# Kernel tuning notes

Hardware: AMD Instinct MI355X
Metric: run time of the kernel (lower is better)

The kernel has to match this reference:

```python
import jax, jax.numpy as jnp
import numpy as np

E = 1024  # embedding_size
H = 16    # num_heads
D = E // H  # head_size = 64
SCALE = 1.0 / np.sqrt(np.float32(E))  # NOTE: original scales by sqrt(embedding_size), not head_size


def setup_inputs() -> dict:
    key = jax.random.key(0)
    ks = jax.random.split(key, 11)
    B, S = 2, 2048
    init = 1.0 / np.sqrt(np.float32(E))
    inp = {
        'q': jax.random.normal(ks[0], (B, S, E), dtype=jnp.float32),
        'k': jax.random.normal(ks[1], (B, S, E), dtype=jnp.float32),
        'v': jax.random.normal(ks[2], (B, S, E), dtype=jnp.float32),
        'wq': jax.random.normal(ks[3], (E, E), dtype=jnp.float32) * init,
        'bq': jax.random.normal(ks[4], (E,), dtype=jnp.float32) * init,
        'wk': jax.random.normal(ks[5], (E, E), dtype=jnp.float32) * init,
        'bk': jax.random.normal(ks[6], (E,), dtype=jnp.float32) * init,
        'wv': jax.random.normal(ks[7], (E, E), dtype=jnp.float32) * init,
        'bv': jax.random.normal(ks[8], (E,), dtype=jnp.float32) * init,
        'wo': jax.random.normal(ks[9], (E, E), dtype=jnp.float32) * init,
        'bo': jax.random.normal(ks[10], (E,), dtype=jnp.float32) * init,
    }
    return inp


def reference(q, k, v, wq, bq, wk, bk, wv, bv, wo, bo):
    S = q.shape[1]
    # Linear projections (torch Linear: x @ W.T + b)
    qp = (q @ wq.T + bq).reshape(-1, H, S, D)  # faithful raw view, not transpose
    kp = (k @ wk.T + bk).reshape(-1, H, S, D)
    vp = (v @ wv.T + bv).reshape(-1, H, S, D)
    # scores / sqrt(embedding_size) -- faithful to original (uses E, not D)
    scores = jnp.einsum('bhqd,bhkd->bhqk', qp, kp) * SCALE
    attn = jax.nn.softmax(scores, axis=-1)  # [B,H,S,S]
    out = jnp.einsum('bhqk,bhkd->bhqd', attn, vp)  # [B,H,S,D]
    out = out.reshape(-1, S, E)
    # dropout is eval-mode identity
    return out @ wo.T + bo
```

## Files before the change

kernel.cpp:

```cpp
#include <hip/hip_runtime.h>
#include <hip/hip_bf16.h>
#include <cstdint>


typedef __bf16 bf16_t;
typedef bf16_t bf16x8 __attribute__((ext_vector_type(8)));
typedef bf16_t bf16x4 __attribute__((ext_vector_type(4)));
typedef float  f32x4  __attribute__((ext_vector_type(4)));
typedef float  f32x16 __attribute__((ext_vector_type(16)));
typedef unsigned int u32;
typedef u32 u32x2 __attribute__((ext_vector_type(2)));

#define MFMA16(a, b, c) __builtin_amdgcn_mfma_f32_16x16x32_bf16((a), (b), (c), 0, 0, 0)
#define MFMA32(a, b, c) __builtin_amdgcn_mfma_f32_32x32x16_bf16((a), (b), (c), 0, 0, 0)

#define GLOAD_LDS16(gptr, lptr)                                                      \
  __builtin_amdgcn_global_load_lds(                                                  \
      (const __attribute__((address_space(1))) void*)(gptr),                         \
      (__attribute__((address_space(3))) void*)(lptr), 16, 0, 0)

namespace {
constexpr int kS = 2048, kE = 1024, kD = 64;
constexpr int kM = 4096;
constexpr float kQScale = 0.03125f;
constexpr float kL2E = 1.44269504088896f;
}

__device__ inline u32 pkbf(float a, float b) {
  u32 r;
  asm("v_cvt_pk_bf16_f32 %0, %1, %2" : "=v"(r) : "v"(a), "v"(b));
  return r;
}

__device__ inline bf16x8 make_pfrag(float v0, float v1, float v2, float v3,
                                    float v4, float v5, float v6, float v7) {
  u32 A0 = pkbf(v0, v1), A1 = pkbf(v2, v3);
  u32 B0 = pkbf(v4, v5), B1 = pkbf(v6, v7);
  u32x2 r0 = __builtin_amdgcn_permlane32_swap(A0, B0, false, false);
  u32x2 r1 = __builtin_amdgcn_permlane32_swap(A1, B1, false, false);
  union { u32 w[4]; bf16x8 v; } u;
  u.w[0] = r0[0]; u.w[1] = r1[0]; u.w[2] = r0[1]; u.w[3] = r1[1];
  return u.v;
}

__global__ void cvt_batch(const float* __restrict__ s0, const float* __restrict__ s1,
                          const float* __restrict__ s2, const float* __restrict__ s3,
                          bf16_t* __restrict__ d0, bf16_t* __restrict__ d1,
                          bf16_t* __restrict__ d2, bf16_t* __restrict__ d3, int n4) {
  const float* s; bf16_t* d;
  switch (blockIdx.y) {
    case 0:  s = s0; d = d0; break;
    case 1:  s = s1; d = d1; break;
    case 2:  s = s2; d = d2; break;
    default: s = s3; d = d3; break;
  }
  int stride = gridDim.x * blockDim.x;
  for (int i = blockIdx.x * blockDim.x + threadIdx.x; i < n4; i += stride) {
    float4 v = reinterpret_cast<const float4*>(s)[i];
    bf16x4 o;
    o[0] = (bf16_t)v.x; o[1] = (bf16_t)v.y; o[2] = (bf16_t)v.z; o[3] = (bf16_t)v.w;
    reinterpret_cast<bf16x4*>(d)[i] = o;
  }
}

__global__ __launch_bounds__(256, 2)
void gemm_qkv(const bf16_t* __restrict__ qb, const bf16_t* __restrict__ kb,
              const bf16_t* __restrict__ vb, const bf16_t* __restrict__ W,
              const float* __restrict__ bq, const float* __restrict__ bk,
              const float* __restrict__ bv,
              bf16_t* __restrict__ Qp, bf16_t* __restrict__ Kp, bf16_t* __restrict__ Vp) {
  constexpr int K = kE, BK = 64;
  __shared__ __align__(16) bf16_t As[128 * BK];
  __shared__ __align__(16) bf16_t Bs[128 * BK];
  const int tid = threadIdx.x, lane = tid & 63, wave = tid >> 6;
  const int fr = lane & 15, fg = lane >> 4;
  const int region = blockIdx.x >> 3;
  const int bm = blockIdx.y * 128, bn = blockIdx.x * 128;
  const int bnl = (blockIdx.x & 7) * 128;
  const bf16_t* A = region == 0 ? qb : region == 1 ? kb : vb;
  const float* bias = region == 0 ? bq : region == 1 ? bk : bv;
  bf16_t* Cp = region == 0 ? Qp : region == 1 ? Kp : Vp;
  const float scale = region == 0 ? kQScale : 1.0f;
  const int wr = (wave >> 1) * 64, wc = (wave & 1) * 64;
  f32x4 acc[4][4] = {};
  for (int k0 = 0; k0 < K; k0 += BK) {
#pragma unroll
    for (int c = 0; c < 4; ++c) {
      int lin = c * 256 + tid, row = lin >> 3, ch = lin & 7, sch = ch ^ (row & 7);
      GLOAD_LDS16(A + (size_t)(bm + row) * K + k0 + sch * 8, (char*)As + lin * 16);
    }
#pragma unroll
    for (int c = 0; c < 4; ++c) {
      int lin = c * 256 + tid, row = lin >> 3, ch = lin & 7, sch = ch ^ (row & 7);
      GLOAD_LDS16(W + (size_t)(bn + row) * K + k0 + sch * 8, (char*)Bs + lin * 16);
    }
    __syncthreads();
#pragma unroll
    for (int kk = 0; kk < 2; ++kk) {
      bf16x8 af[4], bfv[4];
#pragma unroll
      for (int i = 0; i < 4; ++i) {
        int row = wr + i * 16 + fr;
        int ch = (kk * 4 + fg) ^ (row & 7);
        af[i] = *reinterpret_cast<const bf16x8*>((const char*)As + row * 128 + ch * 16);
      }
#pragma unroll
      for (int j = 0; j < 4; ++j) {
        int row = wc + j * 16 + fr;
        int ch = (kk * 4 + fg) ^ (row & 7);
        bfv[j] = *reinterpret_cast<const bf16x8*>((const char*)Bs + row * 128 + ch * 16);
      }
#pragma unroll
      for (int i = 0; i < 4; ++i)
#pragma unroll
        for (int j = 0; j < 4; ++j)
          acc[i][j] = MFMA16(af[i], bfv[j], acc[i][j]);
    }
    __syncthreads();
  }
#pragma unroll
  for (int i = 0; i < 4; ++i)
#pragma unroll
    for (int j = 0; j < 4; ++j) {
      int coll = bnl + wc + j * 16 + fr;
      float bvv = bias[coll];
#pragma unroll
      for (int r = 0; r < 4; ++r) {
        int row = bm + wr + i * 16 + fg * 4 + r;
        Cp[(size_t)row * kE + coll] = (bf16_t)((acc[i][j][r] + bvv) * scale);
      }
    }
}

__global__ __launch_bounds__(256, 2)
void gemm_out(const bf16_t* __restrict__ A, const bf16_t* __restrict__ Bm,
              const float* __restrict__ bias, float* __restrict__ Cout) {
  constexpr int K = kE, BK = 64;
  __shared__ __align__(16) bf16_t As[128 * BK];
  __shared__ __align__(16) bf16_t Bs[64 * BK];
  const int tid = threadIdx.x, lane = tid & 63, wave = tid >> 6;
  const int fr = lane & 15, fg = lane >> 4;
  const int bm = blockIdx.y * 128, bn = blockIdx.x * 64;
  const int wr = wave * 32;
  f32x4 acc[2][4] = {};
  for (int k0 = 0; k0 < K; k0 += BK) {
#pragma unroll
    for (int c = 0; c < 4; ++c) {
      int lin = c * 256 + tid, row = lin >> 3, ch = lin & 7, sch = ch ^ (row & 7);
      GLOAD_LDS16(A + (size_t)(bm + row) * K + k0 + sch * 8, (char*)As + lin * 16);
    }
#pragma unroll
    for (int c = 0; c < 2; ++c) {
      int lin = c * 256 + tid, row = lin >> 3, ch = lin & 7, sch = ch ^ (row & 7);
      GLOAD_LDS16(Bm + (size_t)(bn + row) * K + k0 + sch * 8, (char*)Bs + lin * 16);
    }
    __syncthreads();
#pragma unroll
    for (int kk = 0; kk < 2; ++kk) {
      bf16x8 af[2], bfv[4];
#pragma unroll
      for (int i = 0; i < 2; ++i) {
        int row = wr + i * 16 + fr;
        int ch = (kk * 4 + fg) ^ (row & 7);
        af[i] = *reinterpret_cast<const bf16x8*>((const char*)As + row * 128 + ch * 16);
      }
#pragma unroll
      for (int j = 0; j < 4; ++j) {
        int row = bn - bn + j * 16 + fr;
        int ch = (kk * 4 + fg) ^ (row & 7);
        bfv[j] = *reinterpret_cast<const bf16x8*>((const char*)Bs + row * 128 + ch * 16);
      }
#pragma unroll
      for (int i = 0; i < 2; ++i)
#pragma unroll
        for (int j = 0; j < 4; ++j)
          acc[i][j] = MFMA16(af[i], bfv[j], acc[i][j]);
    }
    __syncthreads();
  }
#pragma unroll
  for (int i = 0; i < 2; ++i)
#pragma unroll
    for (int j = 0; j < 4; ++j) {
      int col = bn + j * 16 + fr;
      float bvv = bias[col];
#pragma unroll
      for (int r = 0; r < 4; ++r) {
        int row = bm + wr + i * 16 + fg * 4 + r;
        Cout[(size_t)row * kE + col] = acc[i][j][r] + bvv;
      }
    }
}

__global__ __launch_bounds__(256)
void vtranspose(const bf16_t* __restrict__ Vp, bf16_t* __restrict__ VpT) {
  __shared__ __align__(16) bf16_t T[256 * 64];
  const int tid = threadIdx.x;
  const size_t hb = (size_t)blockIdx.y * (kS * kD);
  const bf16_t* src = Vp + hb + (size_t)blockIdx.x * 256 * kD;
  bf16_t* dst = VpT + hb + blockIdx.x * 256;
#pragma unroll
  for (int c = 0; c < 8; ++c) {
    int lin = c * 256 + tid;
    int row = lin >> 3, ch = lin & 7;
    bf16x8 v = *reinterpret_cast<const bf16x8*>(src + row * kD + ch * 8);
    *reinterpret_cast<bf16x8*>((char*)T + row * 128 + ((ch ^ ((row >> 3) & 7)) * 16)) = v;
  }
  __syncthreads();
#pragma unroll
  for (int c = 0; c < 8; ++c) {
    int lin = c * 256 + tid;
    int d = lin >> 5, kc = lin & 31;
    bf16x8 o;
#pragma unroll
    for (int e = 0; e < 8; ++e) {
      int s = kc * 8 + e;
      o[e] = *reinterpret_cast<const bf16_t*>(
          (const char*)T + s * 128 + (((d >> 3) ^ ((s >> 3) & 7)) * 16) + (d & 7) * 2);
    }
    *reinterpret_cast<bf16x8*>(dst + (size_t)d * kS + kc * 8) = o;
  }
}

__global__ __launch_bounds__(256, 3)
void attn_fwd(const bf16_t* __restrict__ Qp, const bf16_t* __restrict__ Kp,
              const bf16_t* __restrict__ VpT, bf16_t* __restrict__ Op) {
  __shared__ __align__(16) char smem[32768];
  const int tid = threadIdx.x, lane = tid & 63, wave = tid >> 6;
  const int ql = lane & 31, hi = lane >> 5;
  const int newb = (blockIdx.x & 7) * 64 + (blockIdx.x >> 3);
  const int head = newb >> 4, qt = newb & 15;
  const size_t hbase = (size_t)head * (kS * kD);
  const int q0 = qt * 128 + wave * 32;

  bf16x8 qf[4];
#pragma unroll
  for (int ct = 0; ct < 4; ++ct)
    qf[ct] = *reinterpret_cast<const bf16x8*>(
        Qp + hbase + (size_t)(q0 + ql) * kD + ct * 16 + hi * 8);

  float m = -3.0e38f, Lp = 0.0f;
  f32x16 o0 = {}, o1 = {};

  {
    const bf16_t* Kt = Kp + hbase;
    const bf16_t* Vt = VpT + hbase;
#pragma unroll
    for (int c = 0; c < 2; ++c) {
      int lin = c * 256 + tid, row = lin >> 3, ch = lin & 7, sch = ch ^ (row & 7);
      GLOAD_LDS16(Kt + row * kD + sch * 8, smem + lin * 16);
      GLOAD_LDS16(Vt + (size_t)row * kS + sch * 8, smem + 8192 + lin * 16);
    }
  }

  for (int kt = 0; kt < kS / 64; ++kt) {
    __syncthreads();
    const int cb = (kt & 1) * 16384;
    if (kt + 1 < kS / 64) {
      const int nb = ((kt + 1) & 1) * 16384;
      const bf16_t* Kt = Kp + hbase + (size_t)(kt + 1) * 64 * kD;
      const bf16_t* Vt = VpT + hbase + (kt + 1) * 64;
#pragma unroll
      for (int c = 0; c < 2; ++c) {
        int lin = c * 256 + tid, row = lin >> 3, ch = lin & 7, sch = ch ^ (row & 7);
        GLOAD_LDS16(Kt + row * kD + sch * 8, smem + nb + lin * 16);
        GLOAD_LDS16(Vt + (size_t)row * kS + sch * 8, smem + nb + 8192 + lin * 16);
      }
    }

    f32x16 s0 = {}, s1 = {};
#pragma unroll
    for (int ct = 0; ct < 4; ++ct) {
      bf16x8 k0 = *reinterpret_cast<const bf16x8*>(
          smem + cb + ql * 128 + (((2 * ct + hi) ^ (ql & 7)) * 16));
      bf16x8 k1 = *reinterpret_cast<const bf16x8*>(
          smem + cb + (32 + ql) * 128 + (((2 * ct + hi) ^ (ql & 7)) * 16));
      s0 = MFMA32(k0, qf[ct], s0);
      s1 = MFMA32(k1, qf[ct], s1);
    }

    float t0 = -3.0e38f, t1 = -3.0e38f, t2 = -3.0e38f, t3 = -3.0e38f;
#pragma unroll
    for (int r = 0; r < 16; r += 4) {
      t0 = fmaxf(t0, fmaxf(s0[r], s0[r + 1])); t1 = fmaxf(t1, fmaxf(s0[r + 2], s0[r + 3]));
      t2 = fmaxf(t2, fmaxf(s1[r], s1[r + 1])); t3 = fmaxf(t3, fmaxf(s1[r + 2], s1[r + 3]));
    }
    float tm = fmaxf(fmaxf(t0, t1), fmaxf(t2, t3));
    tm = fmaxf(tm, __shfl_xor(tm, 32));
    if (!__all(tm <= m + 8.0f)) {
      float mn = fmaxf(m, tm);
      float rs = __builtin_amdgcn_exp2f((m - mn) * kL2E);
      m = mn; Lp *= rs;
#pragma unroll
      for (int r = 0; r < 16; ++r) { o0[r] *= rs; o1[r] *= rs; }
    }
    const float ml = m * kL2E;
    float a0 = 0.f, a1 = 0.f;
#pragma unroll
    for (int r = 0; r < 16; ++r) {
      s0[r] = __builtin_amdgcn_exp2f(__builtin_fmaf(s0[r], kL2E, -ml));
      s1[r] = __builtin_amdgcn_exp2f(__builtin_fmaf(s1[r], kL2E, -ml));
      a0 += s0[r]; a1 += s1[r];
    }
    Lp += a0 + a1;

    bf16x8 pf[4];
    pf[0] = make_pfrag(s0[0], s0[1], s0[2], s0[3], s0[4], s0[5], s0[6], s0[7]);
    pf[1] = make_pfrag(s0[8], s0[9], s0[10], s0[11], s0[12], s0[13], s0[14], s0[15]);
    pf[2] = make_pfrag(s1[0], s1[1], s1[2], s1[3], s1[4], s1[5], s1[6], s1[7]);
    pf[3] = make_pfrag(s1[8], s1[9], s1[10], s1[11], s1[12], s1[13], s1[14], s1[15]);

#pragma unroll
    for (int ks = 0; ks < 4; ++ks) {
      bf16x8 v0 = *reinterpret_cast<const bf16x8*>(
          smem + cb + 8192 + ql * 128 + (((2 * ks + hi) ^ (ql & 7)) * 16));
      bf16x8 v1 = *reinterpret_cast<const bf16x8*>(
          smem + cb + 8192 + (32 + ql) * 128 + (((2 * ks + hi) ^ (ql & 7)) * 16));
      o0 = MFMA32(v0, pf[ks], o0);
      o1 = MFMA32(v1, pf[ks], o1);
    }
  }

  float L = Lp + __shfl_xor(Lp, 32);
  float inv = 1.0f / L;
#pragma unroll
  for (int r = 0; r < 16; ++r) { o0[r] *= inv; o1[r] *= inv; }
  const int wb = wave * 4096;
#pragma unroll
  for (int c = 0; c < 4; ++c) {
    {
      u32 w0 = pkbf(o0[4 * c + 0], o0[4 * c + 1]);
      u32 w1 = pkbf(o0[4 * c + 2], o0[4 * c + 3]);
      int d0 = 8 * c + 4 * hi;
      int byte = (wb + ql * 128 + d0 * 2) ^ ((ql & 7) << 4);
      *reinterpret_cast<u32x2*>(smem + byte) = (u32x2){w0, w1};
    }
    {
      u32 w0 = pkbf(o1[4 * c + 0], o1[4 * c + 1]);
      u32 w1 = pkbf(o1[4 * c + 2], o1[4 * c + 3]);
      int d0 = 32 + 8 * c + 4 * hi;
      int byte = (wb + ql * 128 + d0 * 2) ^ ((ql & 7) << 4);
      *reinterpret_cast<u32x2*>(smem + byte) = (u32x2){w0, w1};
    }
  }
  asm volatile("s_waitcnt lgkmcnt(0)" ::: "memory");
  __builtin_amdgcn_sched_barrier(0);
#pragma unroll
  for (int it = 0; it < 4; ++it) {
    int lin = it * 64 + lane;
    int qr = lin >> 3, ch = lin & 7;
    int byte = wb + qr * 128 + ((ch * 16) ^ ((qr & 7) << 4));
    bf16x8 vrow = *reinterpret_cast<const bf16x8*>(smem + byte);
    *reinterpret_cast<bf16x8*>(Op + hbase + (size_t)(q0 + qr) * kD + ch * 8) = vrow;
  }
}

extern "C" void kernel_launch(void* const* d_in, const int* in_sizes, int n_in,
                              void* d_out, int out_size, void* d_ws, size_t ws_size,
                              hipStream_t stream) {
  (void)in_sizes; (void)n_in; (void)out_size; (void)ws_size;
  const float* q  = (const float*)d_in[0];
  const float* k  = (const float*)d_in[1];
  const float* v  = (const float*)d_in[2];
  const float* wq = (const float*)d_in[3];
  const float* bq = (const float*)d_in[4];
  const float* wk = (const float*)d_in[5];
  const float* bk = (const float*)d_in[6];
  const float* wv = (const float*)d_in[7];
  const float* bv = (const float*)d_in[8];
  const float* wo = (const float*)d_in[9];
  const float* bo = (const float*)d_in[10];
  float* out = (float*)d_out;

  char* ws = (char*)d_ws;
  const size_t MB = 1ull << 20;
  bf16_t* qb   = (bf16_t*)(ws +  0 * MB);
  bf16_t* kb   = (bf16_t*)(ws +  8 * MB);
  bf16_t* vb   = (bf16_t*)(ws + 16 * MB);
  bf16_t* wqkv = (bf16_t*)(ws + 24 * MB);
  bf16_t* wob  = (bf16_t*)(ws + 30 * MB);
  bf16_t* Qp   = (bf16_t*)(ws + 32 * MB);
  bf16_t* Kp   = (bf16_t*)(ws + 40 * MB);
  bf16_t* Vp   = (bf16_t*)(ws + 48 * MB);
  bf16_t* Opb  = (bf16_t*)(ws + 56 * MB);
  bf16_t* VpT  = (bf16_t*)(ws +  0 * MB);

  const int nQKV4 = (kM * kE) / 4;
  const int nW4 = (kE * kE) / 4;
  cvt_batch<<<dim3(512, 3), 256, 0, stream>>>(q, k, v, v, qb, kb, vb, vb, nQKV4);
  cvt_batch<<<dim3(128, 4), 256, 0, stream>>>(wq, wk, wv, wo, wqkv, wqkv + 1048576,
                                              wqkv + 2097152, wob, nW4);

  gemm_qkv<<<dim3(24, 32), 256, 0, stream>>>(qb, kb, vb, wqkv, bq, bk, bv, Qp, Kp, Vp);

  vtranspose<<<dim3(kS / 256, 32), 256, 0, stream>>>(Vp, VpT);

  attn_fwd<<<dim3(512), 256, 0, stream>>>(Qp, Kp, VpT, Opb);

  gemm_out<<<dim3(16, 32), 256, 0, stream>>>(Opb, wob, bo, out);
}
```

Measured before the change: 128.1 us.

## Software-pipeline attention so PV of previous tile overlaps QK of current

Restructures the attention main loop so the P·V MFMAs for tile kt-1 are issued alongside the Q·K MFMAs for tile kt, with P fragments ping-ponged between two register sets and K/V staged in separate double buffers. The goal is to hide softmax exp and permute latency behind matrix work, and s_setprio raises priority around the MFMA section. Blocks shrink to two waves (64 query rows) with twice as many blocks, and the cross-half shuffles become permlane32_swap. The trade-offs are more register pressure from the extra P fragments, a loose launch-bounds hint, and more K reloads across the larger block count.

```diff
diff --git a/kernel.cpp b/kernel.cpp
--- a/kernel.cpp
+++ b/kernel.cpp
@@ -41,6 +41,17 @@
   union { u32 w[4]; bf16x8 v; } u;
   u.w[0] = r0[0]; u.w[1] = r1[0]; u.w[2] = r0[1]; u.w[3] = r1[1];
   return u.v;
+}
+
+__device__ inline float xhalf_max(float x) {
+  u32 xu = __builtin_bit_cast(u32, x);
+  u32x2 r = __builtin_amdgcn_permlane32_swap(xu, xu, false, false);
+  return fmaxf(__builtin_bit_cast(float, r[0]), __builtin_bit_cast(float, r[1]));
+}
+__device__ inline float xhalf_sum(float x) {
+  u32 xu = __builtin_bit_cast(u32, x);
+  u32x2 r = __builtin_amdgcn_permlane32_swap(xu, xu, false, false);
+  return __builtin_bit_cast(float, r[0]) + __builtin_bit_cast(float, r[1]);
 }
 
 __global__ void cvt_batch(const float* __restrict__ s0, const float* __restrict__ s1,
@@ -166,7 +177,7 @@
       }
 #pragma unroll
       for (int j = 0; j < 4; ++j) {
-        int row = bn - bn + j * 16 + fr;
+        int row = j * 16 + fr;
         int ch = (kk * 4 + fg) ^ (row & 7);
         bfv[j] = *reinterpret_cast<const bf16x8*>((const char*)Bs + row * 128 + ch * 16);
       }
@@ -222,16 +233,94 @@
   }
 }
 
-__global__ __launch_bounds__(256, 3)
+#define ATTN_BODY(KT, PFW, PFR, DOPV, STAGEK)                                        \
+  {                                                                                  \
+    __syncthreads();                                                                 \
+    const int cb = ((KT) & 1) * 8192;                                                \
+    const int vbR = 16384 + ((((KT) + 1) & 1) * 8192);                               \
+    if (STAGEK) {                                                                    \
+      const bf16_t* Ktp = Kp + hbase + (size_t)((KT) + 1) * 64 * kD;                 \
+      const int nb = (((KT) + 1) & 1) * 8192;                                        \
+      _Pragma("unroll")                                                              \
+      for (int c = 0; c < 4; ++c) {                                                  \
+        int lin = c * 128 + tid, row = lin >> 3, ch = lin & 7, sch = ch ^ (row & 7); \
+        GLOAD_LDS16(Ktp + row * kD + sch * 8, smem + nb + lin * 16);                 \
+      }                                                                              \
+    }                                                                                \
+    {                                                                                \
+      const bf16_t* Vtp = VpT + hbase + (KT) * 64;                                   \
+      const int vbW = 16384 + (((KT) & 1) * 8192);                                   \
+      _Pragma("unroll")                                                              \
+      for (int c = 0; c < 4; ++c) {                                                  \
+        int lin = c * 128 + tid, row = lin >> 3, ch = lin & 7, sch = ch ^ (row & 7); \
+        GLOAD_LDS16(Vtp + (size_t)row * kS + sch * 8, smem + vbW + lin * 16);        \
+      }                                                                              \
+    }                                                                                \
+    f32x16 s0 = {}, s1 = {};                                                         \
+    __builtin_amdgcn_s_setprio(1);                                                   \
+    _Pragma("unroll")                                                                \
+    for (int ct = 0; ct < 4; ++ct) {                                                 \
+      bf16x8 k0 = *reinterpret_cast<const bf16x8*>(                                  \
+          smem + cb + ql * 128 + (((2 * ct + hi) ^ (ql & 7)) * 16));                 \
+      bf16x8 k1 = *reinterpret_cast<const bf16x8*>(                                  \
+          smem + cb + (32 + ql) * 128 + (((2 * ct + hi) ^ (ql & 7)) * 16));          \
+      s0 = MFMA32(k0, qf[ct], s0);                                                   \
+      s1 = MFMA32(k1, qf[ct], s1);                                                   \
+    }                                                                                \
+    if (DOPV) {                                                                      \
+      _Pragma("unroll")                                                              \
+      for (int ks = 0; ks < 4; ++ks) {                                               \
+        bf16x8 v0 = *reinterpret_cast<const bf16x8*>(                                \
+            smem + vbR + ql * 128 + (((2 * ks + hi) ^ (ql & 7)) * 16));              \
+        bf16x8 v1 = *reinterpret_cast<const bf16x8*>(                                \
+            smem + vbR + (32 + ql) * 128 + (((2 * ks + hi) ^ (ql & 7)) * 16));       \
+        o0 = MFMA32(v0, PFR[ks], o0);                                                \
+        o1 = MFMA32(v1, PFR[ks], o1);                                                \
+      }                                                                              \
+    }                                                                                \
+    __builtin_amdgcn_s_setprio(0);                                                   \
+    float t0 = -3.0e38f, t1 = -3.0e38f, t2 = -3.0e38f, t3 = -3.0e38f;                \
+    _Pragma("unroll")                                                                \
+    for (int r = 0; r < 16; r += 4) {                                                \
+      t0 = fmaxf(t0, fmaxf(s0[r], s0[r + 1]));                                       \
+      t1 = fmaxf(t1, fmaxf(s0[r + 2], s0[r + 3]));                                   \
+      t2 = fmaxf(t2, fmaxf(s1[r], s1[r + 1]));                                       \
+      t3 = fmaxf(t3, fmaxf(s1[r + 2], s1[r + 3]));                                   \
+    }                                                                                \
+    float tm = fmaxf(fmaxf(t0, t1), fmaxf(t2, t3));                                  \
+    tm = xhalf_max(tm);                                                              \
+    if (!__all(tm <= m + 8.0f)) {                                                    \
+      float mn = fmaxf(m, tm);                                                       \
+      float rs = __builtin_amdgcn_exp2f((m - mn) * kL2E);                            \
+      m = mn; Lp *= rs;                                                              \
+      _Pragma("unroll")                                                              \
+      for (int r = 0; r < 16; ++r) { o0[r] *= rs; o1[r] *= rs; }                     \
+    }                                                                                \
+    const float ml = m * kL2E;                                                       \
+    float a0 = 0.f, a1 = 0.f;                                                        \
+    _Pragma("unroll")                                                                \
+    for (int r = 0; r < 16; ++r) {                                                   \
+      s0[r] = __builtin_amdgcn_exp2f(__builtin_fmaf(s0[r], kL2E, -ml));              \
+      s1[r] = __builtin_amdgcn_exp2f(__builtin_fmaf(s1[r], kL2E, -ml));              \
+      a0 += s0[r]; a1 += s1[r];                                                      \
+    }                                                                                \
+    Lp += a0 + a1;                                                                   \
+    PFW[0] = make_pfrag(s0[0], s0[1], s0[2], s0[3], s0[4], s0[5], s0[6], s0[7]);     \
+    PFW[1] = make_pfrag(s0[8], s0[9], s0[10], s0[11], s0[12], s0[13], s0[14], s0[15]);\
+    PFW[2] = make_pfrag(s1[0], s1[1], s1[2], s1[3], s1[4], s1[5], s1[6], s1[7]);     \
+    PFW[3] = make_pfrag(s1[8], s1[9], s1[10], s1[11], s1[12], s1[13], s1[14], s1[15]);\
+  }
+
+__global__ __launch_bounds__(128, 2)
 void attn_fwd(const bf16_t* __restrict__ Qp, const bf16_t* __restrict__ Kp,
               const bf16_t* __restrict__ VpT, bf16_t* __restrict__ Op) {
   __shared__ __align__(16) char smem[32768];
   const int tid = threadIdx.x, lane = tid & 63, wave = tid >> 6;
   const int ql = lane & 31, hi = lane >> 5;
-  const int newb = (blockIdx.x & 7) * 64 + (blockIdx.x >> 3);
-  const int head = newb >> 4, qt = newb & 15;
+  const int newb = ((int)blockIdx.x & 7) * 128 + ((int)blockIdx.x >> 3);
+  const int head = newb >> 5, qt = newb & 31;
   const size_t hbase = (size_t)head * (kS * kD);
-  const int q0 = qt * 128 + wave * 32;
+  const int q0 = qt * 64 + wave * 32;
 
   bf16x8 qf[4];
 #pragma unroll
@@ -241,87 +330,38 @@
 
   float m = -3.0e38f, Lp = 0.0f;
   f32x16 o0 = {}, o1 = {};
+  bf16x8 pfA[4], pfB[4];
 
   {
-    const bf16_t* Kt = Kp + hbase;
-    const bf16_t* Vt = VpT + hbase;
-#pragma unroll
-    for (int c = 0; c < 2; ++c) {
-      int lin = c * 256 + tid, row = lin >> 3, ch = lin & 7, sch = ch ^ (row & 7);
-      GLOAD_LDS16(Kt + row * kD + sch * 8, smem + lin * 16);
-      GLOAD_LDS16(Vt + (size_t)row * kS + sch * 8, smem + 8192 + lin * 16);
-    }
-  }
-
-  for (int kt = 0; kt < kS / 64; ++kt) {
-    __syncthreads();
-    const int cb = (kt & 1) * 16384;
-    if (kt + 1 < kS / 64) {
-      const int nb = ((kt + 1) & 1) * 16384;
-      const bf16_t* Kt = Kp + hbase + (size_t)(kt + 1) * 64 * kD;
-      const bf16_t* Vt = VpT + hbase + (kt + 1) * 64;
-#pragma unroll
-      for (int c = 0; c < 2; ++c) {
-        int lin = c * 256 + tid, row = lin >> 3, ch = lin & 7, sch = ch ^ (row & 7);
-        GLOAD_LDS16(Kt + row * kD + sch * 8, smem + nb + lin * 16);
-        GLOAD_LDS16(Vt + (size_t)row * kS + sch * 8, smem + nb + 8192 + lin * 16);
-      }
-    }
-
-    f32x16 s0 = {}, s1 = {};
-#pragma unroll
-    for (int ct = 0; ct < 4; ++ct) {
-      bf16x8 k0 = *reinterpret_cast<const bf16x8*>(
-          smem + cb + ql * 128 + (((2 * ct + hi) ^ (ql & 7)) * 16));
-      bf16x8 k1 = *reinterpret_cast<const bf16x8*>(
-          smem + cb + (32 + ql) * 128 + (((2 * ct + hi) ^ (ql & 7)) * 16));
-      s0 = MFMA32(k0, qf[ct], s0);
-      s1 = MFMA32(k1, qf[ct], s1);
-    }
-
-    float t0 = -3.0e38f, t1 = -3.0e38f, t2 = -3.0e38f, t3 = -3.0e38f;
-#pragma unroll
-    for (int r = 0; r < 16; r += 4) {
-      t0 = fmaxf(t0, fmaxf(s0[r], s0[r + 1])); t1 = fmaxf(t1, fmaxf(s0[r + 2], s0[r + 3]));
-      t2 = fmaxf(t2, fmaxf(s1[r], s1[r + 1])); t3 = fmaxf(t3, fmaxf(s1[r + 2], s1[r + 3]));
-    }
-    float tm = fmaxf(fmaxf(t0, t1), fmaxf(t2, t3));
-    tm = fmaxf(tm, __shfl_xor(tm, 32));
-    if (!__all(tm <= m + 8.0f)) {
-      float mn = fmaxf(m, tm);
-      float rs = __builtin_amdgcn_exp2f((m - mn) * kL2E);
-      m = mn; Lp *= rs;
-#pragma unroll
-      for (int r = 0; r < 16; ++r) { o0[r] *= rs; o1[r] *= rs; }
-    }
-    const float ml = m * kL2E;
-    float a0 = 0.f, a1 = 0.f;
-#pragma unroll
-    for (int r = 0; r < 16; ++r) {
-      s0[r] = __builtin_amdgcn_exp2f(__builtin_fmaf(s0[r], kL2E, -ml));
-      s1[r] = __builtin_amdgcn_exp2f(__builtin_fmaf(s1[r], kL2E, -ml));
-      a0 += s0[r]; a1 += s1[r];
-    }
-    Lp += a0 + a1;
-
-    bf16x8 pf[4];
-    pf[0] = make_pfrag(s0[0], s0[1], s0[2], s0[3], s0[4], s0[5], s0[6], s0[7]);
-    pf[1] = make_pfrag(s0[8], s0[9], s0[10], s0[11], s0[12], s0[13], s0[14], s0[15]);
-    pf[2] = make_pfrag(s1[0], s1[1], s1[2], s1[3], s1[4], s1[5], s1[6], s1[7]);
-    pf[3] = make_pfrag(s1[8], s1[9], s1[10], s1[11], s1[12], s1[13], s1[14], s1[15]);
-
-#pragma unroll
-    for (int ks = 0; ks < 4; ++ks) {
-      bf16x8 v0 = *reinterpret_cast<const bf16x8*>(
-          smem + cb + 8192 + ql * 128 + (((2 * ks + hi) ^ (ql & 7)) * 16));
-      bf16x8 v1 = *reinterpret_cast<const bf16x8*>(
-          smem + cb + 8192 + (32 + ql) * 128 + (((2 * ks + hi) ^ (ql & 7)) * 16));
-      o0 = MFMA32(v0, pf[ks], o0);
-      o1 = MFMA32(v1, pf[ks], o1);
-    }
-  }
-
-  float L = Lp + __shfl_xor(Lp, 32);
+    const bf16_t* Ktp = Kp + hbase;
+#pragma unroll
+    for (int c = 0; c < 4; ++c) {
+      int lin = c * 128 + tid, row = lin >> 3, ch = lin & 7, sch = ch ^ (row & 7);
+      GLOAD_LDS16(Ktp + row * kD + sch * 8, smem + lin * 16);
+    }
+  }
+
+  ATTN_BODY(0, pfA, pfB, false, true)
+#pragma unroll 1
+  for (int it = 0; it < 15; ++it) {
+    const int kt = 1 + 2 * it;
+    ATTN_BODY(kt, pfB, pfA, true, true)
+    ATTN_BODY(kt + 1, pfA, pfB, true, true)
+  }
+  ATTN_BODY(31, pfB, pfA, true, false)
+
+  __syncthreads();
+#pragma unroll
+  for (int ks = 0; ks < 4; ++ks) {
+    bf16x8 v0 = *reinterpret_cast<const bf16x8*>(
+        smem + 24576 + ql * 128 + (((2 * ks + hi) ^ (ql & 7)) * 16));
+    bf16x8 v1 = *reinterpret_cast<const bf16x8*>(
+        smem + 24576 + (32 + ql) * 128 + (((2 * ks + hi) ^ (ql & 7)) * 16));
+    o0 = MFMA32(v0, pfB[ks], o0);
+    o1 = MFMA32(v1, pfB[ks], o1);
+  }
+
+  float L = xhalf_sum(Lp);
   float inv = 1.0f / L;
 #pragma unroll
   for (int r = 0; r < 16; ++r) { o0[r] *= inv; o1[r] *= inv; }
@@ -395,7 +435,7 @@
 
   vtranspose<<<dim3(kS / 256, 32), 256, 0, stream>>>(Vp, VpT);
 
-  attn_fwd<<<dim3(512), 256, 0, stream>>>(Qp, Kp, VpT, Opb);
+  attn_fwd<<<dim3(1024), 128, 0, stream>>>(Qp, Kp, VpT, Opb);
 
   gemm_out<<<dim3(16, 32), 256, 0, stream>>>(Opb, wob, bo, out);
 }
```

After: 134.8 us. +5.3%, slower.

## Restructure attention to single-wave blocks loading K/V directly into registers

Applied to the files above, without the earlier changes.

Attention now runs one 64-thread wave per block over 2048 blocks. Each wave loads K and V fragments straight from global memory into registers with a two-stage register double buffer, replacing the shared LDS double buffer and block-wide barriers. The half-wave max and sum reductions use permlane32_swap instead of shuffles, and s_setprio is raised around the MFMA groups. This removes LDS traffic and __syncthreads but drops K/V reuse across waves, so each wave reads K/V from L2 on its own, and register pressure goes up.

```diff
diff --git a/kernel.cpp b/kernel.cpp
--- a/kernel.cpp
+++ b/kernel.cpp
@@ -41,6 +41,17 @@
   union { u32 w[4]; bf16x8 v; } u;
   u.w[0] = r0[0]; u.w[1] = r1[0]; u.w[2] = r0[1]; u.w[3] = r1[1];
   return u.v;
+}
+
+__device__ inline float xhalf_max(float x) {
+  u32 xu = __builtin_bit_cast(u32, x);
+  u32x2 r = __builtin_amdgcn_permlane32_swap(xu, xu, false, false);
+  return fmaxf(__builtin_bit_cast(float, r[0]), __builtin_bit_cast(float, r[1]));
+}
+__device__ inline float xhalf_sum(float x) {
+  u32 xu = __builtin_bit_cast(u32, x);
+  u32x2 r = __builtin_amdgcn_permlane32_swap(xu, xu, false, false);
+  return __builtin_bit_cast(float, r[0]) + __builtin_bit_cast(float, r[1]);
 }
 
 __global__ void cvt_batch(const float* __restrict__ s0, const float* __restrict__ s1,
@@ -166,7 +177,7 @@
       }
 #pragma unroll
       for (int j = 0; j < 4; ++j) {
-        int row = bn - bn + j * 16 + fr;
+        int row = j * 16 + fr;
         int ch = (kk * 4 + fg) ^ (row & 7);
         bfv[j] = *reinterpret_cast<const bf16x8*>((const char*)Bs + row * 128 + ch * 16);
       }
@@ -222,16 +233,75 @@
   }
 }
 
-__global__ __launch_bounds__(256, 3)
+#define LOADK(dst, T)                                                          \
+  _Pragma("unroll") for (int g = 0; g < 2; ++g)                                \
+  _Pragma("unroll") for (int ct = 0; ct < 4; ++ct)                             \
+      dst[g * 4 + ct] = *reinterpret_cast<const bf16x8*>(                      \
+          Kb + (size_t)(T) * (64 * kD) + (g * 32 + ql) * kD + ct * 16 + hi * 8);
+
+#define LOADV(dst, T)                                                          \
+  _Pragma("unroll") for (int g = 0; g < 2; ++g)                                \
+  _Pragma("unroll") for (int ks = 0; ks < 4; ++ks)                             \
+      dst[g * 4 + ks] = *reinterpret_cast<const bf16x8*>(                      \
+          Vb + (size_t)(g * 32 + ql) * kS + (T) * 64 + ks * 16 + hi * 8);
+
+#define ATTN_COMPUTE(kf, vf)                                                   \
+  {                                                                            \
+    f32x16 s0 = {}, s1 = {};                                                   \
+    __builtin_amdgcn_s_setprio(1);                                             \
+    _Pragma("unroll") for (int ct = 0; ct < 4; ++ct) {                         \
+      s0 = MFMA32(kf[ct], qf[ct], s0);                                         \
+      s1 = MFMA32(kf[4 + ct], qf[ct], s1);                                     \
+    }                                                                          \
+    __builtin_amdgcn_s_setprio(0);                                             \
+    float t0 = -3.0e38f, t1 = -3.0e38f, t2 = -3.0e38f, t3 = -3.0e38f;          \
+    _Pragma("unroll") for (int r = 0; r < 16; r += 4) {                        \
+      t0 = fmaxf(t0, fmaxf(s0[r], s0[r + 1]));                                 \
+      t1 = fmaxf(t1, fmaxf(s0[r + 2], s0[r + 3]));                             \
+      t2 = fmaxf(t2, fmaxf(s1[r], s1[r + 1]));                                 \
+      t3 = fmaxf(t3, fmaxf(s1[r + 2], s1[r + 3]));                             \
+    }                                                                          \
+    float tm = fmaxf(fmaxf(t0, t1), fmaxf(t2, t3));                            \
+    tm = xhalf_max(tm);                                                        \
+    if (!__all(tm <= m + 8.0f)) {                                              \
+      float mn = fmaxf(m, tm);                                                 \
+      float rs = __builtin_amdgcn_exp2f((m - mn) * kL2E);                      \
+      m = mn; Lp *= rs;                                                        \
+      _Pragma("unroll") for (int r = 0; r < 16; ++r) { o0[r] *= rs; o1[r] *= rs; } \
+    }                                                                          \
+    const float ml = m * kL2E;                                                 \
+    float a0 = 0.f, a1 = 0.f;                                                  \
+    _Pragma("unroll") for (int r = 0; r < 16; ++r) {                           \
+      s0[r] = __builtin_amdgcn_exp2f(__builtin_fmaf(s0[r], kL2E, -ml));        \
+      s1[r] = __builtin_amdgcn_exp2f(__builtin_fmaf(s1[r], kL2E, -ml));        \
+      a0 += s0[r]; a1 += s1[r];                                                \
+    }                                                                          \
+    Lp += a0 + a1;                                                             \
+    bf16x8 pf0 = make_pfrag(s0[0], s0[1], s0[2], s0[3], s0[4], s0[5], s0[6], s0[7]); \
+    bf16x8 pf1 = make_pfrag(s0[8], s0[9], s0[10], s0[11], s0[12], s0[13], s0[14], s0[15]); \
+    bf16x8 pf2 = make_pfrag(s1[0], s1[1], s1[2], s1[3], s1[4], s1[5], s1[6], s1[7]); \
+    bf16x8 pf3 = make_pfrag(s1[8], s1[9], s1[10], s1[11], s1[12], s1[13], s1[14], s1[15]); \
+    __builtin_amdgcn_s_setprio(1);                                             \
+    o0 = MFMA32(vf[0], pf0, o0); o1 = MFMA32(vf[4], pf0, o1);                  \
+    o0 = MFMA32(vf[1], pf1, o0); o1 = MFMA32(vf[5], pf1, o1);                  \
+    o0 = MFMA32(vf[2], pf2, o0); o1 = MFMA32(vf[6], pf2, o1);                  \
+    o0 = MFMA32(vf[3], pf3, o0); o1 = MFMA32(vf[7], pf3, o1);                  \
+    __builtin_amdgcn_s_setprio(0);                                             \
+  }
+
+__global__ __launch_bounds__(64, 2)
 void attn_fwd(const bf16_t* __restrict__ Qp, const bf16_t* __restrict__ Kp,
               const bf16_t* __restrict__ VpT, bf16_t* __restrict__ Op) {
-  __shared__ __align__(16) char smem[32768];
-  const int tid = threadIdx.x, lane = tid & 63, wave = tid >> 6;
+  __shared__ __align__(16) char smem[8192];
+  const int lane = threadIdx.x & 63;
   const int ql = lane & 31, hi = lane >> 5;
-  const int newb = (blockIdx.x & 7) * 64 + (blockIdx.x >> 3);
-  const int head = newb >> 4, qt = newb & 15;
+  const int newb = ((int)blockIdx.x & 7) * 256 + ((int)blockIdx.x >> 3);
+  const int head = newb >> 6, qt = newb & 63;
   const size_t hbase = (size_t)head * (kS * kD);
-  const int q0 = qt * 128 + wave * 32;
+  const int q0 = qt * 32;
+
+  const bf16_t* Kb = Kp + hbase;
+  const bf16_t* Vb = VpT + hbase;
 
   bf16x8 qf[4];
 #pragma unroll
@@ -241,105 +311,40 @@
 
   float m = -3.0e38f, Lp = 0.0f;
   f32x16 o0 = {}, o1 = {};
-
-  {
-    const bf16_t* Kt = Kp + hbase;
-    const bf16_t* Vt = VpT + hbase;
-#pragma unroll
-    for (int c = 0; c < 2; ++c) {
-      int lin = c * 256 + tid, row = lin >> 3, ch = lin & 7, sch = ch ^ (row & 7);
-      GLOAD_LDS16(Kt + row * kD + sch * 8, smem + lin * 16);
-      GLOAD_LDS16(Vt + (size_t)row * kS + sch * 8, smem + 8192 + lin * 16);
-    }
-  }
-
-  for (int kt = 0; kt < kS / 64; ++kt) {
-    __syncthreads();
-    const int cb = (kt & 1) * 16384;
-    if (kt + 1 < kS / 64) {
-      const int nb = ((kt + 1) & 1) * 16384;
-      const bf16_t* Kt = Kp + hbase + (size_t)(kt + 1) * 64 * kD;
-      const bf16_t* Vt = VpT + hbase + (kt + 1) * 64;
-#pragma unroll
-      for (int c = 0; c < 2; ++c) {
-        int lin = c * 256 + tid, row = lin >> 3, ch = lin & 7, sch = ch ^ (row & 7);
-        GLOAD_LDS16(Kt + row * kD + sch * 8, smem + nb + lin * 16);
-        GLOAD_LDS16(Vt + (size_t)row * kS + sch * 8, smem + nb + 8192 + lin * 16);
-      }
-    }
-
-    f32x16 s0 = {}, s1 = {};
-#pragma unroll
-    for (int ct = 0; ct < 4; ++ct) {
-      bf16x8 k0 = *reinterpret_cast<const bf16x8*>(
-          smem + cb + ql * 128 + (((2 * ct + hi) ^ (ql & 7)) * 16));
-      bf16x8 k1 = *reinterpret_cast<const bf16x8*>(
-          smem + cb + (32 + ql) * 128 + (((2 * ct + hi) ^ (ql & 7)) * 16));
-      s0 = MFMA32(k0, qf[ct], s0);
-      s1 = MFMA32(k1, qf[ct], s1);
-    }
-
-    float t0 = -3.0e38f, t1 = -3.0e38f, t2 = -3.0e38f, t3 = -3.0e38f;
-#pragma unroll
-    for (int r = 0; r < 16; r += 4) {
-      t0 = fmaxf(t0, fmaxf(s0[r], s0[r + 1])); t1 = fmaxf(t1, fmaxf(s0[r + 2], s0[r + 3]));
-      t2 = fmaxf(t2, fmaxf(s1[r], s1[r + 1])); t3 = fmaxf(t3, fmaxf(s1[r + 2], s1[r + 3]));
-    }
-    float tm = fmaxf(fmaxf(t0, t1), fmaxf(t2, t3));
-    tm = fmaxf(tm, __shfl_xor(tm, 32));
-    if (!__all(tm <= m + 8.0f)) {
-      float mn = fmaxf(m, tm);
-      float rs = __builtin_amdgcn_exp2f((m - mn) * kL2E);
-      m = mn; Lp *= rs;
-#pragma unroll
-      for (int r = 0; r < 16; ++r) { o0[r] *= rs; o1[r] *= rs; }
-    }
-    const float ml = m * kL2E;
-    float a0 = 0.f, a1 = 0.f;
-#pragma unroll
-    for (int r = 0; r < 16; ++r) {
-      s0[r] = __builtin_amdgcn_exp2f(__builtin_fmaf(s0[r], kL2E, -ml));
-      s1[r] = __builtin_amdgcn_exp2f(__builtin_fmaf(s1[r], kL2E, -ml));
-      a0 += s0[r]; a1 += s1[r];
-    }
-    Lp += a0 + a1;
-
-    bf16x8 pf[4];
-    pf[0] = make_pfrag(s0[0], s0[1], s0[2], s0[3], s0[4], s0[5], s0[6], s0[7]);
-    pf[1] = make_pfrag(s0[8], s0[9], s0[10], s0[11], s0[12], s0[13], s0[14], s0[15]);
-    pf[2] = make_pfrag(s1[0], s1[1], s1[2], s1[3], s1[4], s1[5], s1[6], s1[7]);
-    pf[3] = make_pfrag(s1[8], s1[9], s1[10], s1[11], s1[12], s1[13], s1[14], s1[15]);
-
-#pragma unroll
-    for (int ks = 0; ks < 4; ++ks) {
-      bf16x8 v0 = *reinterpret_cast<const bf16x8*>(
-          smem + cb + 8192 + ql * 128 + (((2 * ks + hi) ^ (ql & 7)) * 16));
-      bf16x8 v1 = *reinterpret_cast<const bf16x8*>(
-          smem + cb + 8192 + (32 + ql) * 128 + (((2 * ks + hi) ^ (ql & 7)) * 16));
-      o0 = MFMA32(v0, pf[ks], o0);
-      o1 = MFMA32(v1, pf[ks], o1);
-    }
-  }
-
-  float L = Lp + __shfl_xor(Lp, 32);
+  bf16x8 kA[8], vA[8], kB[8], vB[8];
+
+  LOADK(kA, 0)
+  LOADV(vA, 0)
+#pragma unroll 1
+  for (int it = 0; it < 16; ++it) {
+    const int t = 2 * it;
+    LOADK(kB, t + 1)
+    LOADV(vB, t + 1)
+    ATTN_COMPUTE(kA, vA)
+    const int tn = (t + 2 < 32) ? (t + 2) : 31;
+    LOADK(kA, tn)
+    LOADV(vA, tn)
+    ATTN_COMPUTE(kB, vB)
+  }
+
+  float L = xhalf_sum(Lp);
   float inv = 1.0f / L;
 #pragma unroll
   for (int r = 0; r < 16; ++r) { o0[r] *= inv; o1[r] *= inv; }
-  const int wb = wave * 4096;
 #pragma unroll
   for (int c = 0; c < 4; ++c) {
     {
       u32 w0 = pkbf(o0[4 * c + 0], o0[4 * c + 1]);
       u32 w1 = pkbf(o0[4 * c + 2], o0[4 * c + 3]);
       int d0 = 8 * c + 4 * hi;
-      int byte = (wb + ql * 128 + d0 * 2) ^ ((ql & 7) << 4);
+      int byte = (ql * 128 + d0 * 2) ^ ((ql & 7) << 4);
       *reinterpret_cast<u32x2*>(smem + byte) = (u32x2){w0, w1};
     }
     {
       u32 w0 = pkbf(o1[4 * c + 0], o1[4 * c + 1]);
       u32 w1 = pkbf(o1[4 * c + 2], o1[4 * c + 3]);
       int d0 = 32 + 8 * c + 4 * hi;
-      int byte = (wb + ql * 128 + d0 * 2) ^ ((ql & 7) << 4);
+      int byte = (ql * 128 + d0 * 2) ^ ((ql & 7) << 4);
       *reinterpret_cast<u32x2*>(smem + byte) = (u32x2){w0, w1};
     }
   }
@@ -349,7 +354,7 @@
   for (int it = 0; it < 4; ++it) {
     int lin = it * 64 + lane;
     int qr = lin >> 3, ch = lin & 7;
-    int byte = wb + qr * 128 + ((ch * 16) ^ ((qr & 7) << 4));
+    int byte = qr * 128 + ((ch * 16) ^ ((qr & 7) << 4));
     bf16x8 vrow = *reinterpret_cast<const bf16x8*>(smem + byte);
     *reinterpret_cast<bf16x8*>(Op + hbase + (size_t)(q0 + qr) * kD + ch * 8) = vrow;
   }
@@ -395,7 +400,7 @@
 
   vtranspose<<<dim3(kS / 256, 32), 256, 0, stream>>>(Vp, VpT);
 
-  attn_fwd<<<dim3(512), 256, 0, stream>>>(Qp, Kp, VpT, Opb);
+  attn_fwd<<<dim3(2048), 64, 0, stream>>>(Qp, Kp, VpT, Opb);
 
   gemm_out<<<dim3(16, 32), 256, 0, stream>>>(Opb, wob, bo, out);
 }
```

New measurement: 197.6 us. 1.54x slower.
